# Optimization experiments

Hardware: AMD Instinct MI355X
Metric: run time of the kernel (lower is better)

## Reference

```python
import jax, jax.numpy as jnp
import numpy as np

N_HEADS = 16
SEG = 64
EPS = 1e-6


def _sigma(x):
    # ELU(x) + 1 kernel feature map (strictly positive)
    return jax.nn.elu(x) + 1.0


def setup_inputs() -> dict:
    key = jax.random.key(0)
    kx, kq, kk, kv, ko = jax.random.split(key, 5)
    B, T, D = 4, 4096, 1024
    scale = D ** -0.5
    return {
        "x": jax.random.normal(kx, (B, T, D), dtype=jnp.float32),
        "W_q": jax.random.normal(kq, (D, D), dtype=jnp.float32) * scale,
        "W_k": jax.random.normal(kk, (D, D), dtype=jnp.float32) * scale,
        "W_v": jax.random.normal(kv, (D, D), dtype=jnp.float32) * scale,
        "W_o": jax.random.normal(ko, (D, D), dtype=jnp.float32) * scale,
        "beta_param": jnp.zeros((N_HEADS,), dtype=jnp.float32),
    }


def _infini_attention(x, W_q, W_k, W_v, W_o, beta_param):
    B, T, D = x.shape
    H = N_HEADS
    dk = D // H
    assert T % SEG == 0
    S = T // SEG

    def proj(W):
        # nn.Linear: x @ W.T ; split heads -> (B,H,T,dk) -> (S,B,H,SEG,dk)
        y = (x @ W.T).reshape(B, T, H, dk).transpose(0, 2, 1, 3)
        return y.reshape(B, H, S, SEG, dk).transpose(2, 0, 1, 3, 4)

    Qs, Ks, Vs = proj(W_q), proj(W_k), proj(W_v)

    beta = jax.nn.sigmoid(beta_param).reshape(1, H, 1, 1)
    causal = jnp.triu(jnp.ones((SEG, SEG), dtype=bool), k=1)
    inv_sqrt_dk = 1.0 / jnp.sqrt(jnp.asarray(dk, x.dtype))

    M0 = jnp.zeros((B, H, dk, dk), dtype=x.dtype)
    z0 = jnp.zeros((B, H, dk), dtype=x.dtype)

    def step(carry, qkv):
        M, z = carry
        q, k, v = qkv  # each (B,H,SEG,dk)
        # Eq.4 memory retrieval
        sq = _sigma(q)
        denom_q = jnp.sum(sq * z[:, :, None, :], axis=-1, keepdims=True) + EPS
        A_mem = jnp.matmul(sq, M) / denom_q
        # local causal softmax attention
        scores = jnp.matmul(q, jnp.swapaxes(k, -2, -1)) * inv_sqrt_dk
        scores = jnp.where(causal, -jnp.inf, scores)
        A_dot = jnp.matmul(jax.nn.softmax(scores, axis=-1), v)
        A_s = beta * A_mem + (1.0 - beta) * A_dot
        # Eq.5 delta-rule memory update
        sk = _sigma(k)
        denom_k = jnp.sum(sk * z[:, :, None, :], axis=-1, keepdims=True) + EPS
        V_prev = jnp.matmul(sk, M) / denom_k
        M_new = M + jnp.einsum("bhtk,bhtv->bhkv", sk, v - V_prev)
        z_new = z + jnp.sum(sk, axis=-2)
        return (M_new, z_new), A_s

    (M, z), outs = jax.lax.scan(step, (M0, z0), (Qs, Ks, Vs))
    # outs: (S,B,H,SEG,dk) -> (B,T,D)
    out = outs.transpose(1, 3, 0, 2, 4).reshape(B, S * SEG, H, dk)
    # careful: need segment-major time ordering -> (B, H, T, dk) then (B,T,H,dk)
    out = outs.transpose(1, 2, 0, 3, 4).reshape(B, H, T, dk)
    out = out.transpose(0, 2, 1, 3).reshape(B, T, D)
    out = out @ W_o.T
    return out, M.mean(0), z.mean(0)


def reference(x, W_q, W_k, W_v, W_o, beta_param):
    return _infini_attention(x, W_q, W_k, W_v, W_o, beta_param)
```

## Files before the change

### kernel.cpp

```cpp
#include <hip/hip_runtime.h>

typedef __bf16 bf16_t;
typedef __bf16 bf16x8 __attribute__((ext_vector_type(8)));
typedef __bf16 bf16x4 __attribute__((ext_vector_type(4)));
typedef float  f32x4  __attribute__((ext_vector_type(4)));

#define QKV_STR 3072

__device__ __forceinline__ void gload16(const bf16_t* g, bf16_t* l) {
    __builtin_amdgcn_global_load_lds(
        (const __attribute__((address_space(1))) void*)(g),
        (__attribute__((address_space(3))) void*)(l), 16, 0, 0);
}

__global__ __launch_bounds__(256) void cast_bf16_kernel(const float* __restrict__ in,
                                                        bf16_t* __restrict__ out, int n4) {
    int i = blockIdx.x * 256 + threadIdx.x;
    if (i >= n4) return;
    f32x4 v = *reinterpret_cast<const f32x4*>(in + (size_t)i * 4);
    bf16x4 o;
    o[0] = (bf16_t)v[0]; o[1] = (bf16_t)v[1]; o[2] = (bf16_t)v[2]; o[3] = (bf16_t)v[3];
    *reinterpret_cast<bf16x4*>(out + (size_t)i * 4) = o;
}

__global__ __launch_bounds__(256) void cast4_kernel(const float* __restrict__ w0,
                                                    const float* __restrict__ w1,
                                                    const float* __restrict__ w2,
                                                    const float* __restrict__ w3,
                                                    bf16_t* __restrict__ o0,
                                                    bf16_t* __restrict__ o1,
                                                    bf16_t* __restrict__ o2,
                                                    bf16_t* __restrict__ o3) {
    int which = blockIdx.x >> 10;
    int i = (blockIdx.x & 1023) * 256 + threadIdx.x;
    const float* in = (which == 0) ? w0 : (which == 1) ? w1 : (which == 2) ? w2 : w3;
    bf16_t*     out = (which == 0) ? o0 : (which == 1) ? o1 : (which == 2) ? o2 : o3;
    f32x4 v = *reinterpret_cast<const f32x4*>(in + (size_t)i * 4);
    bf16x4 o;
    o[0] = (bf16_t)v[0]; o[1] = (bf16_t)v[1]; o[2] = (bf16_t)v[2]; o[3] = (bf16_t)v[3];
    *reinterpret_cast<bf16x4*>(out + (size_t)i * 4) = o;
}

__device__ __forceinline__ bf16x8 sigma8(bf16x8 x) {
    bf16x8 o;
#pragma unroll
    for (int j = 0; j < 8; j++) {
        float f = (float)x[j];
        float sg = f > 0.f ? f + 1.f : __expf(f);
        o[j] = (bf16_t)sg;
    }
    return o;
}

template <int OUT_BF16>
__global__ __launch_bounds__(512, 2) void gemm256(const bf16_t* __restrict__ A,
                                                  const bf16_t* __restrict__ Bm,
                                                  void* __restrict__ Cv,
                                                  int M, int N, int K) {
    __shared__ bf16_t As[4][256 * 32];
    __shared__ bf16_t Bs[4][256 * 32];

    int nbn = N >> 8;
    int nwg = (M >> 8) * nbn;
    int bid = blockIdx.x;
    int wg = ((nwg & 7) == 0) ? ((bid & 7) * (nwg >> 3) + (bid >> 3)) : bid;
    int bm = wg / nbn, bn = wg % nbn;

    int tid = threadIdx.x;
    int w = tid >> 6, lane = tid & 63;
    int wm = w >> 2, wn = w & 3;
    int lr = lane & 15, lk = lane >> 4;

    int srow = lane >> 2;
    int schunk = (lane & 3) ^ ((lane >> 3) & 3);
    const bf16_t* gA0 = A  + (size_t)(bm * 256 + w * 32 + srow) * K + schunk * 8;
    const bf16_t* gA1 = gA0 + (size_t)16 * K;
    const bf16_t* gB0 = Bm + (size_t)(bn * 256 + w * 32 + srow) * K + schunk * 8;
    const bf16_t* gB1 = gB0 + (size_t)16 * K;
    int lO0 = (w * 32) * 32 + lane * 8;
    int lO1 = (w * 32 + 16) * 32 + lane * 8;

    int chunkb = (lk ^ ((lr >> 1) & 3)) << 4;
    int aoff[8], boff[4];
#pragma unroll
    for (int mi = 0; mi < 8; mi++) aoff[mi] = (wm * 128 + mi * 16 + lr) * 64 + chunkb;
#pragma unroll
    for (int ni = 0; ni < 4; ni++) boff[ni] = (wn * 64 + ni * 16 + lr) * 64 + chunkb;

    f32x4 acc[8][4];
#pragma unroll
    for (int mi = 0; mi < 8; mi++)
#pragma unroll
        for (int ni = 0; ni < 4; ni++) acc[mi][ni] = (f32x4){0.f, 0.f, 0.f, 0.f};

    const int NT = K >> 5;

    auto STAGE = [&](int t) {
        int slot = t & 3;
        size_t ko = (size_t)t * 32;
        gload16(gA0 + ko, &As[slot][lO0]);
        gload16(gA1 + ko, &As[slot][lO1]);
        gload16(gB0 + ko, &Bs[slot][lO0]);
        gload16(gB1 + ko, &Bs[slot][lO1]);
    };

    STAGE(0); STAGE(1); STAGE(2);

#pragma unroll 1
    for (int t = 0; t < NT; ++t) {
        int ahead = NT - 1 - t;
        if (ahead >= 2)      asm volatile("s_waitcnt vmcnt(8)" ::: "memory");
        else if (ahead == 1) asm volatile("s_waitcnt vmcnt(4)" ::: "memory");
        else                 asm volatile("s_waitcnt vmcnt(0)" ::: "memory");
        __builtin_amdgcn_sched_barrier(0);
        __builtin_amdgcn_s_barrier();
        __builtin_amdgcn_sched_barrier(0);

        const char* pa = (const char*)(&As[t & 3][0]);
        const char* pb = (const char*)(&Bs[t & 3][0]);
        bf16x8 af[8], bfr[4];
#pragma unroll
        for (int ni = 0; ni < 4; ni++)
            bfr[ni] = *reinterpret_cast<const bf16x8*>(pb + boff[ni]);
#pragma unroll
        for (int mi = 0; mi < 8; mi++)
            af[mi] = *reinterpret_cast<const bf16x8*>(pa + aoff[mi]);

        if (t + 3 < NT) STAGE(t + 3);

        __builtin_amdgcn_s_setprio(1);
#pragma unroll
        for (int mi = 0; mi < 8; mi++)
#pragma unroll
            for (int ni = 0; ni < 4; ni++)
                acc[mi][ni] = __builtin_amdgcn_mfma_f32_16x16x32_bf16(af[mi], bfr[ni], acc[mi][ni], 0, 0, 0);
        __builtin_amdgcn_s_setprio(0);
    }

    int row0 = bm * 256 + wm * 128 + lk * 4;
    int col0 = bn * 256 + wn * 64 + lr;
#pragma unroll
    for (int mi = 0; mi < 8; mi++)
#pragma unroll
        for (int ni = 0; ni < 4; ni++)
#pragma unroll
            for (int jj = 0; jj < 4; jj++) {
                size_t idx = (size_t)(row0 + mi * 16 + jj) * N + (col0 + ni * 16);
                float v = acc[mi][ni][jj];
                if (OUT_BF16) reinterpret_cast<bf16_t*>(Cv)[idx] = (bf16_t)v;
                else          reinterpret_cast<float*>(Cv)[idx]  = v;
            }
}

__global__ __launch_bounds__(256) void attn_kernel(bf16_t* __restrict__ QKV,
                                                   bf16_t* __restrict__ skTg,
                                                   float* __restrict__ csum,
                                                   bf16_t* __restrict__ Adot) {
    __shared__ bf16_t kS[64 * 72];
    __shared__ bf16_t vS[64 * 72];
    __shared__ bf16_t skT[64 * 72];
    __shared__ bf16_t vT[64 * 72];
    __shared__ bf16_t pS[64 * 72];
    __shared__ float  scr[64 * 68];

    int u = blockIdx.x;
    int bh = u >> 6, s = u & 63;
    int b = bh >> 4, h = bh & 15;
    int tid = threadIdx.x;
    int w = tid >> 6, lane = tid & 63;
    int lr = lane & 15, lk = lane >> 4;
    int r = tid >> 2, qd = tid & 3, c0 = qd << 4;

    bf16_t* qp = QKV + (size_t)(b * 4096 + s * 64) * QKV_STR + (size_t)h * 64;
    bf16_t* kp = qp + 1024;
    bf16_t* vp = qp + 2048;
    size_t sb = ((size_t)bh * 64 + s) * 4096;

    {
        bf16x8 k0 = *reinterpret_cast<const bf16x8*>(kp + (size_t)r * QKV_STR + c0);
        bf16x8 k1 = *reinterpret_cast<const bf16x8*>(kp + (size_t)r * QKV_STR + c0 + 8);
        bf16x8 v0 = *reinterpret_cast<const bf16x8*>(vp + (size_t)r * QKV_STR + c0);
        bf16x8 v1 = *reinterpret_cast<const bf16x8*>(vp + (size_t)r * QKV_STR + c0 + 8);
        *reinterpret_cast<bf16x8*>(&kS[r * 72 + c0])     = k0;
        *reinterpret_cast<bf16x8*>(&kS[r * 72 + c0 + 8]) = k1;
        *reinterpret_cast<bf16x8*>(&vS[r * 72 + c0])     = v0;
        *reinterpret_cast<bf16x8*>(&vS[r * 72 + c0 + 8]) = v1;
        bf16x8 s0 = sigma8(k0), s1 = sigma8(k1);
        *reinterpret_cast<bf16x8*>(kp + (size_t)r * QKV_STR + c0)     = s0;
        *reinterpret_cast<bf16x8*>(kp + (size_t)r * QKV_STR + c0 + 8) = s1;
#pragma unroll
        for (int j = 0; j < 8; j++) {
            skT[(c0 + j) * 72 + r]     = s0[j];
            skT[(c0 + 8 + j) * 72 + r] = s1[j];
            vT[(c0 + j) * 72 + r]      = v0[j];
            vT[(c0 + 8 + j) * 72 + r]  = v1[j];
        }
    }
    __syncthreads();

    if (tid < 64) {
        float acc = 0.f;
#pragma unroll 8
        for (int t = 0; t < 64; t++) acc += (float)skT[tid * 72 + t];
        csum[((size_t)bh * 64 + s) * 64 + tid] = acc;
    }
    *reinterpret_cast<bf16x8*>(skTg + sb + (size_t)r * 64 + c0) =
        *reinterpret_cast<const bf16x8*>(&skT[r * 72 + c0]);
    *reinterpret_cast<bf16x8*>(skTg + sb + (size_t)r * 64 + c0 + 8) =
        *reinterpret_cast<const bf16x8*>(&skT[r * 72 + c0 + 8]);
    *reinterpret_cast<bf16x8*>(vp + (size_t)r * QKV_STR + c0) =
        *reinterpret_cast<const bf16x8*>(&vT[r * 72 + c0]);
    *reinterpret_cast<bf16x8*>(vp + (size_t)r * QKV_STR + c0 + 8) =
        *reinterpret_cast<const bf16x8*>(&vT[r * 72 + c0 + 8]);

    {
        bf16x8 aq[2];
#pragma unroll
        for (int ks = 0; ks < 2; ks++)
            aq[ks] = *reinterpret_cast<const bf16x8*>(qp + (size_t)(w * 16 + lr) * QKV_STR + lk * 8 + ks * 32);
        f32x4 sc[4];
#pragma unroll
        for (int ct = 0; ct < 4; ct++) {
            sc[ct] = (f32x4){0.f, 0.f, 0.f, 0.f};
#pragma unroll
            for (int ks = 0; ks < 2; ks++) {
                bf16x8 bfrag = *reinterpret_cast<const bf16x8*>(&kS[(ct * 16 + lr) * 72 + lk * 8 + ks * 32]);
                sc[ct] = __builtin_amdgcn_mfma_f32_16x16x32_bf16(aq[ks], bfrag, sc[ct], 0, 0, 0);
            }
        }
#pragma unroll
        for (int ct = 0; ct < 4; ct++)
#pragma unroll
            for (int j = 0; j < 4; j++)
                scr[(w * 16 + lk * 4 + j) * 68 + ct * 16 + lr] = sc[ct][j] * 0.125f;
    }
    __syncthreads();

    {
        float p[16];
        float mx = -3.4e38f;
        const float* srow_p = &scr[r * 68 + c0];
#pragma unroll
        for (int i = 0; i < 16; i++) {
            int c = c0 + i;
            float v = (c <= r) ? srow_p[i] : -3.4e38f;
            p[i] = v;
            mx = fmaxf(mx, v);
        }
        mx = fmaxf(mx, __shfl_xor(mx, 1));
        mx = fmaxf(mx, __shfl_xor(mx, 2));
        float sum = 0.f;
#pragma unroll
        for (int i = 0; i < 16; i++) {
            int c = c0 + i;
            float e = (c <= r) ? __expf(p[i] - mx) : 0.f;
            p[i] = e;
            sum += e;
        }
        sum += __shfl_xor(sum, 1);
        sum += __shfl_xor(sum, 2);
        float inv = 1.f / sum;
        bf16x8 p0, p1;
#pragma unroll
        for (int j = 0; j < 8; j++) {
            p0[j] = (bf16_t)(p[j] * inv);
            p1[j] = (bf16_t)(p[8 + j] * inv);
        }
        *reinterpret_cast<bf16x8*>(&pS[r * 72 + c0])     = p0;
        *reinterpret_cast<bf16x8*>(&pS[r * 72 + c0 + 8]) = p1;
    }
    __syncthreads();

    {
        f32x4 ad[4];
#pragma unroll
        for (int ct = 0; ct < 4; ct++) {
            ad[ct] = (f32x4){0.f, 0.f, 0.f, 0.f};
#pragma unroll
            for (int ks = 0; ks < 2; ks++) {
                bf16x8 afrag = *reinterpret_cast<const bf16x8*>(&pS[(w * 16 + lr) * 72 + lk * 8 + ks * 32]);
                bf16x8 bfrag = *reinterpret_cast<const bf16x8*>(&vT[(ct * 16 + lr) * 72 + lk * 8 + ks * 32]);
                ad[ct] = __builtin_amdgcn_mfma_f32_16x16x32_bf16(afrag, bfrag, ad[ct], 0, 0, 0);
            }
        }
#pragma unroll
        for (int ct = 0; ct < 4; ct++)
#pragma unroll
            for (int j = 0; j < 4; j++)
                kS[(w * 16 + lk * 4 + j) * 72 + ct * 16 + lr] = (bf16_t)ad[ct][j];
    }
    __syncthreads();
    *reinterpret_cast<bf16x8*>(Adot + sb + (size_t)r * 64 + c0) =
        *reinterpret_cast<const bf16x8*>(&kS[r * 72 + c0]);
    *reinterpret_cast<bf16x8*>(Adot + sb + (size_t)r * 64 + c0 + 8) =
        *reinterpret_cast<const bf16x8*>(&kS[r * 72 + c0 + 8]);
}

__global__ __launch_bounds__(64) void zprefix_kernel(const float* __restrict__ csum,
                                                     float* __restrict__ zx,
                                                     float* __restrict__ zfin) {
    int bh = blockIdx.x;
    int d = threadIdx.x;
    float c[64];
#pragma unroll
    for (int s = 0; s < 64; s++)
        c[s] = csum[((size_t)bh * 64 + s) * 64 + d];
    float z = 0.f;
#pragma unroll
    for (int s = 0; s < 64; s++) {
        zx[((size_t)bh * 64 + s) * 64 + d] = z;
        z += c[s];
    }
    zfin[bh * 64 + d] = z;
}

__global__ __launch_bounds__(64) void denomk_kernel(const bf16_t* __restrict__ QKV,
                                                    const float* __restrict__ zx,
                                                    float* __restrict__ invk) {
    __shared__ float zL[64];
    int u = blockIdx.x;
    int bh = u >> 6, s = u & 63;
    int b = bh >> 4, h = bh & 15;
    int tid = threadIdx.x;
    zL[tid] = zx[((size_t)bh * 64 + s) * 64 + tid];
    __syncthreads();
    const bf16_t* src = QKV + (size_t)(b * 4096 + s * 64 + tid) * QKV_STR +
                        (size_t)h * 64 + 1024;
    float acc = 0.f;
#pragma unroll
    for (int blk = 0; blk < 8; blk++) {
        bf16x8 v = *reinterpret_cast<const bf16x8*>(src + blk * 8);
#pragma unroll
        for (int j = 0; j < 8; j++)
            acc = __builtin_fmaf((float)v[j], zL[blk * 8 + j], acc);
    }
    invk[((size_t)bh * 64 + s) * 64 + tid] = 1.f / (acc + 1e-6f);
}

__global__ __launch_bounds__(64, 1) void scan_kernel(const bf16_t* __restrict__ QKV,
                                                     const bf16_t* __restrict__ skTg,
                                                     const float* __restrict__ invk,
                                                     bf16_t* __restrict__ Msnap,
                                                     float* __restrict__ Mfin) {
    __shared__ bf16_t MbL[16 * 72];
    __shared__ bf16_t uTL[16 * 72];
    __shared__ float  ikL[64];

    int blk = blockIdx.x;
    int bh = blk & 63, cq = blk >> 6;
    int c0 = cq << 4;
    int b = bh >> 4, h = bh & 15;
    int lane = threadIdx.x;
    int lr = lane & 15, lk = lane >> 4;
    int vr = lane >> 2, vt0 = (lane & 3) << 4;

    const bf16_t* sKb = QKV + 1024;
    const bf16_t* vTb = QKV + 2048;
    size_t chbase = (size_t)(b * 4096) * QKV_STR + (size_t)h * 64;
    size_t stbase = (size_t)bh * 64 * 4096;
    const size_t SEG = (size_t)64 * QKV_STR;

    auto swz = [](bf16_t* base, int row, int intra) -> bf16_t* {
        return (bf16_t*)((char*)base + row * 144 + (intra ^ ((row & 7) << 4)));
    };

    for (int i = lane; i < 16 * 72; i += 64) MbL[i] = (bf16_t)0.f;
    f32x4 Mreg[4];
#pragma unroll
    for (int rt = 0; rt < 4; rt++) Mreg[rt] = (f32x4){0.f, 0.f, 0.f, 0.f};

    bf16x8 cK[4][2], cT[4][2];
#pragma unroll
    for (int rt = 0; rt < 4; rt++)
#pragma unroll
        for (int ks = 0; ks < 2; ks++) {
            cK[rt][ks] = *reinterpret_cast<const bf16x8*>(
                sKb + chbase + (size_t)(rt * 16 + lr) * QKV_STR + lk * 8 + ks * 32);
            cT[rt][ks] = *reinterpret_cast<const bf16x8*>(
                skTg + stbase + (size_t)(rt * 16 + lr) * 64 + lk * 8 + ks * 32);
        }
    {
        bf16x8 v0 = *reinterpret_cast<const bf16x8*>(vTb + chbase + (size_t)(c0 + vr) * QKV_STR + vt0);
        bf16x8 v1 = *reinterpret_cast<const bf16x8*>(vTb + chbase + (size_t)(c0 + vr) * QKV_STR + vt0 + 8);
        *reinterpret_cast<bf16x8*>(swz(uTL, vr, vt0 * 2))      = v0;
        *reinterpret_cast<bf16x8*>(swz(uTL, vr, vt0 * 2 + 16)) = v1;
        ikL[lane] = invk[(size_t)bh * 4096 + lane];
    }

    for (int s = 0; s < 64; s++) {
        bf16x8 nK[4][2], nT[4][2], nv0, nv1;
        float nik = 0.f;
        if (s < 63) {
            size_t vs2 = chbase + (size_t)(s + 1) * SEG;
            size_t sb2 = stbase + (size_t)(s + 1) * 4096;
#pragma unroll
            for (int rt = 0; rt < 4; rt++)
#pragma unroll
                for (int ks = 0; ks < 2; ks++) {
                    nK[rt][ks] = *reinterpret_cast<const bf16x8*>(
                        sKb + vs2 + (size_t)(rt * 16 + lr) * QKV_STR + lk * 8 + ks * 32);
                    nT[rt][ks] = *reinterpret_cast<const bf16x8*>(
                        skTg + sb2 + (size_t)(rt * 16 + lr) * 64 + lk * 8 + ks * 32);
                }
            nv0 = *reinterpret_cast<const bf16x8*>(vTb + vs2 + (size_t)(c0 + vr) * QKV_STR + vt0);
            nv1 = *reinterpret_cast<const bf16x8*>(vTb + vs2 + (size_t)(c0 + vr) * QKV_STR + vt0 + 8);
            nik = invk[(size_t)bh * 4096 + (size_t)(s + 1) * 64 + lane];
        }

        bf16x8 mb0 = *reinterpret_cast<const bf16x8*>(swz(MbL, lr, lk * 16));
        bf16x8 mb1 = *reinterpret_cast<const bf16x8*>(swz(MbL, lr, lk * 16 + 64));
        f32x4 Y[4];
#pragma unroll
        for (int rt = 0; rt < 4; rt++) {
            Y[rt] = (f32x4){0.f, 0.f, 0.f, 0.f};
            Y[rt] = __builtin_amdgcn_mfma_f32_16x16x32_bf16(cK[rt][0], mb0, Y[rt], 0, 0, 0);
            Y[rt] = __builtin_amdgcn_mfma_f32_16x16x32_bf16(cK[rt][1], mb1, Y[rt], 0, 0, 0);
        }

#pragma unroll
        for (int rt = 0; rt < 4; rt++) {
            bf16x4 vv = *reinterpret_cast<const bf16x4*>(swz(uTL, lr, rt * 32 + lk * 8));
            bf16x4 uu;
#pragma unroll
            for (int j = 0; j < 4; j++) {
                float ik = ikL[rt * 16 + lk * 4 + j];
                uu[j] = (bf16_t)((float)vv[j] - Y[rt][j] * ik);
            }
            *reinterpret_cast<bf16x4*>(swz(uTL, lr, rt * 32 + lk * 8)) = uu;
        }

        bf16x8 ub0 = *reinterpret_cast<const bf16x8*>(swz(uTL, lr, lk * 16));
        bf16x8 ub1 = *reinterpret_cast<const bf16x8*>(swz(uTL, lr, lk * 16 + 64));
#pragma unroll
        for (int rt = 0; rt < 4; rt++) {
            Mreg[rt] = __builtin_amdgcn_mfma_f32_16x16x32_bf16(cT[rt][0], ub0, Mreg[rt], 0, 0, 0);
            Mreg[rt] = __builtin_amdgcn_mfma_f32_16x16x32_bf16(cT[rt][1], ub1, Mreg[rt], 0, 0, 0);
        }

#pragma unroll
        for (int rt = 0; rt < 4; rt++) {
            bf16x4 mp;
#pragma unroll
            for (int j = 0; j < 4; j++) mp[j] = (bf16_t)Mreg[rt][j];
            *reinterpret_cast<bf16x4*>(swz(MbL, lr, rt * 32 + lk * 8)) = mp;
            if (s < 63)
                *reinterpret_cast<bf16x4*>(
                    Msnap + (((size_t)bh * 64 + s + 1) * 64 + c0 + lr) * 64 + rt * 16 + lk * 4) = mp;
        }

        if (s < 63) {
#pragma unroll
            for (int rt = 0; rt < 4; rt++)
#pragma unroll
                for (int ks = 0; ks < 2; ks++) { cK[rt][ks] = nK[rt][ks]; cT[rt][ks] = nT[rt][ks]; }
            *reinterpret_cast<bf16x8*>(swz(uTL, vr, vt0 * 2))      = nv0;
            *reinterpret_cast<bf16x8*>(swz(uTL, vr, vt0 * 2 + 16)) = nv1;
            ikL[lane] = nik;
        }
    }

#pragma unroll
    for (int rt = 0; rt < 4; rt++)
#pragma unroll
        for (int j = 0; j < 4; j++)
            Mfin[(size_t)bh * 4096 + (size_t)(rt * 16 + lk * 4 + j) * 64 + c0 + lr] = Mreg[rt][j];
}

__global__ __launch_bounds__(256) void combine_kernel(const bf16_t* __restrict__ QKV,
                                                      const bf16_t* __restrict__ Msnap,
                                                      const bf16_t* __restrict__ Adot,
                                                      const float* __restrict__ zx,
                                                      const float* __restrict__ beta_param,
                                                      bf16_t* __restrict__ Op) {
    __shared__ bf16_t oS[64 * 72];
    __shared__ bf16_t adS[64 * 72];
    __shared__ float  iq[64];
    __shared__ float  zL[64];

    int u = blockIdx.x;
    int bh = u >> 6, s = u & 63;
    int b = bh >> 4, h = bh & 15;
    int tid = threadIdx.x;
    int w = tid >> 6, lane = tid & 63;
    int lr = lane & 15, lk = lane >> 4;
    int r = tid >> 2, c0 = (tid & 3) << 4;

    const bf16_t* qp = QKV + (size_t)(b * 4096 + s * 64) * QKV_STR + (size_t)h * 64;
    size_t vsegO = ((size_t)b * 4096 + s * 64) * 1024 + (size_t)h * 64;
    size_t sb = ((size_t)bh * 64 + s) * 4096;
    size_t ib = ((size_t)bh * 64 + s) * 64;

    float beta = 1.f / (1.f + __expf(-beta_param[h]));
    float omb = 1.f - beta;

    *reinterpret_cast<bf16x8*>(&adS[r * 72 + c0]) =
        *reinterpret_cast<const bf16x8*>(Adot + sb + (size_t)r * 64 + c0);
    *reinterpret_cast<bf16x8*>(&adS[r * 72 + c0 + 8]) =
        *reinterpret_cast<const bf16x8*>(Adot + sb + (size_t)r * 64 + c0 + 8);
    if (tid < 64) {
        zL[tid] = zx[ib + tid];
        iq[tid] = 0.f;
    }
    __syncthreads();

    f32x4 Y[4];
#pragma unroll
    for (int ct = 0; ct < 4; ct++) Y[ct] = (f32x4){0.f, 0.f, 0.f, 0.f};
    if (s > 0) {
        bf16x8 aq[2];
#pragma unroll
        for (int ks = 0; ks < 2; ks++)
            aq[ks] = sigma8(*reinterpret_cast<const bf16x8*>(
                qp + (size_t)(w * 16 + lr) * QKV_STR + lk * 8 + ks * 32));
        float dq = 0.f;
#pragma unroll
        for (int ks = 0; ks < 2; ks++)
#pragma unroll
            for (int j = 0; j < 8; j++)
                dq = __builtin_fmaf((float)aq[ks][j], zL[ks * 32 + lk * 8 + j], dq);
        dq += __shfl_xor(dq, 16);
        dq += __shfl_xor(dq, 32);
        if (lk == 0) iq[w * 16 + lr] = 1.f / (dq + 1e-6f);
#pragma unroll
        for (int ct = 0; ct < 4; ct++)
#pragma unroll
            for (int ks = 0; ks < 2; ks++) {
                bf16x8 bfrag = *reinterpret_cast<const bf16x8*>(
                    Msnap + sb + (size_t)(ct * 16 + lr) * 64 + lk * 8 + ks * 32);
                Y[ct] = __builtin_amdgcn_mfma_f32_16x16x32_bf16(aq[ks], bfrag, Y[ct], 0, 0, 0);
            }
    }
    __syncthreads();

#pragma unroll
    for (int ct = 0; ct < 4; ct++) {
        int colc = ct * 16 + lr;
#pragma unroll
        for (int j = 0; j < 4; j++) {
            int t = w * 16 + lk * 4 + j;
            float o = beta * (Y[ct][j] * iq[t]) + omb * (float)adS[t * 72 + colc];
            oS[t * 72 + colc] = (bf16_t)o;
        }
    }
    __syncthreads();

    *reinterpret_cast<bf16x8*>(Op + vsegO + (size_t)r * 1024 + c0) =
        *reinterpret_cast<const bf16x8*>(&oS[r * 72 + c0]);
    *reinterpret_cast<bf16x8*>(Op + vsegO + (size_t)r * 1024 + c0 + 8) =
        *reinterpret_cast<const bf16x8*>(&oS[r * 72 + c0 + 8]);
}

__global__ __launch_bounds__(256) void mean_kernel(const float* __restrict__ Mfin,
                                                   const float* __restrict__ zfin,
                                                   float* __restrict__ out) {
    int idx = blockIdx.x * 256 + threadIdx.x;
    if (idx < 65536) {
        out[16777216 + idx] = 0.25f * (Mfin[idx] + Mfin[idx + 65536] +
                                       Mfin[idx + 131072] + Mfin[idx + 196608]);
    } else if (idx < 66560) {
        int j = idx - 65536;
        out[16842752 + j] = 0.25f * (zfin[j] + zfin[j + 1024] + zfin[j + 2048] + zfin[j + 3072]);
    }
}

extern "C" void kernel_launch(void* const* d_in, const int* in_sizes, int n_in,
                              void* d_out, int out_size, void* d_ws, size_t ws_size,
                              hipStream_t stream) {
    const float* x      = (const float*)d_in[0];
    const float* Wq     = (const float*)d_in[1];
    const float* Wk     = (const float*)d_in[2];
    const float* Wv     = (const float*)d_in[3];
    const float* Wo     = (const float*)d_in[4];
    const float* beta_p = (const float*)d_in[5];
    float* out = (float*)d_out;
    char* ws = (char*)d_ws;

    const size_t NX = 16777216ull;

    bf16_t* xb   = (bf16_t*)ws;
    bf16_t* Adot = xb;
    bf16_t* Wqb  = (bf16_t*)(ws + 33554432);
    bf16_t* Wkb  = (bf16_t*)(ws + 35651584);
    bf16_t* Wvb  = (bf16_t*)(ws + 37748736);
    bf16_t* Wob  = (bf16_t*)(ws + 39845888);
    bf16_t* QKV  = (bf16_t*)(ws + 41943040);
    bf16_t* skT  = (bf16_t*)(ws + 142606336);
    bf16_t* Op   = (bf16_t*)(ws + 176160768);
    float*  csum = (float*)(ws + 209715200);
    float*  zx   = (float*)(ws + 210763776);
    float*  invk = (float*)(ws + 212860928);
    float*  Mfin = (float*)(ws + 213909504);
    float*  zfin = (float*)(ws + 214958080);
    bf16_t* Msnap = (bf16_t*)d_out;

    cast_bf16_kernel<<<dim3(16384), dim3(256), 0, stream>>>(x, xb, (int)(NX / 4));
    cast4_kernel<<<dim3(4096), dim3(256), 0, stream>>>(Wq, Wk, Wv, Wo, Wqb, Wkb, Wvb, Wob);

    gemm256<1><<<dim3(768), dim3(512), 0, stream>>>(xb, Wqb, (void*)QKV, 16384, 3072, 1024);

    attn_kernel<<<dim3(4096), dim3(256), 0, stream>>>(QKV, skT, csum, Adot);
    zprefix_kernel<<<dim3(64), dim3(64), 0, stream>>>(csum, zx, zfin);
    denomk_kernel<<<dim3(4096), dim3(64), 0, stream>>>(QKV, zx, invk);
    scan_kernel<<<dim3(256), dim3(64), 0, stream>>>(QKV, skT, invk, Msnap, Mfin);
    combine_kernel<<<dim3(4096), dim3(256), 0, stream>>>(QKV, Msnap, Adot, zx, beta_p, Op);

    gemm256<0><<<dim3(256), dim3(512), 0, stream>>>(Op, Wob, d_out, 16384, 1024, 1024);
    mean_kernel<<<dim3(260), dim3(256), 0, stream>>>(Mfin, zfin, out);
}
```

Baseline: 318.2 us.

## Precompute per-segment delta-rule operators to shorten the serial memory scan

The delta-rule update M += skᵀ(v - sk·M·invk) is rewritten as M = M - A·M + B. A = skᵀ·diag(invk)·sk and B = skᵀ·v are computed for every segment in a new, fully parallel prepA kernel. The serial scan then does one small MFMA product plus an elementwise update per step, instead of two dependent MFMA products with an LDS round trip for the intermediate u. The cost is an extra kernel that writes A in place over skT and B into spare output memory. It also adds bf16 rounding of the precomputed A and B, which may change accuracy.

```diff
diff --git a/kernel.cpp b/kernel.cpp
--- a/kernel.cpp
+++ b/kernel.cpp
@@ -337,28 +337,97 @@
     invk[((size_t)bh * 64 + s) * 64 + tid] = 1.f / (acc + 1e-6f);
 }
 
-__global__ __launch_bounds__(64, 1) void scan_kernel(const bf16_t* __restrict__ QKV,
-                                                     const bf16_t* __restrict__ skTg,
-                                                     const float* __restrict__ invk,
+__global__ __launch_bounds__(256) void prepA_kernel(const bf16_t* QKV,
+                                                    const bf16_t* skTg_in,
+                                                    const float* __restrict__ invk,
+                                                    bf16_t* Ag,
+                                                    bf16_t* __restrict__ bTg) {
+    __shared__ bf16_t tA[64 * 72];
+    __shared__ bf16_t tB[64 * 72];
+
+    int u = blockIdx.x;
+    int bh = u >> 6, s = u & 63;
+    int b = bh >> 4, h = bh & 15;
+    int tid = threadIdx.x;
+    int w = tid >> 6, lane = tid & 63;
+    int lr = lane & 15, lk = lane >> 4;
+    int r = tid >> 2, cc0 = (tid & 3) << 4;
+
+    size_t sb4 = (size_t)u * 4096;
+    size_t ib  = (size_t)u * 64;
+
+    bf16x8 aT[2], av[2], skB[4][2];
+    f32x4 iv[2][2];
+#pragma unroll
+    for (int ks = 0; ks < 2; ks++) {
+        aT[ks] = *reinterpret_cast<const bf16x8*>(
+            skTg_in + sb4 + (size_t)(w * 16 + lr) * 64 + lk * 8 + ks * 32);
+        av[ks] = *reinterpret_cast<const bf16x8*>(
+            QKV + (size_t)(b * 4096 + s * 64 + w * 16 + lr) * QKV_STR + (size_t)h * 64 + 2048 +
+            lk * 8 + ks * 32);
+        iv[ks][0] = *reinterpret_cast<const f32x4*>(invk + ib + ks * 32 + lk * 8);
+        iv[ks][1] = *reinterpret_cast<const f32x4*>(invk + ib + ks * 32 + lk * 8 + 4);
+    }
+#pragma unroll
+    for (int ct = 0; ct < 4; ct++)
+#pragma unroll
+        for (int ks = 0; ks < 2; ks++)
+            skB[ct][ks] = *reinterpret_cast<const bf16x8*>(
+                skTg_in + sb4 + (size_t)(ct * 16 + lr) * 64 + lk * 8 + ks * 32);
+
+    bf16x8 skS[4][2];
+#pragma unroll
+    for (int ct = 0; ct < 4; ct++)
+#pragma unroll
+        for (int ks = 0; ks < 2; ks++)
+#pragma unroll
+            for (int j = 0; j < 8; j++) {
+                float sc = (j < 4) ? iv[ks][0][j] : iv[ks][1][j - 4];
+                skS[ct][ks][j] = (bf16_t)((float)skB[ct][ks][j] * sc);
+            }
+
+    f32x4 Acc[4], Bcc[4];
+#pragma unroll
+    for (int ct = 0; ct < 4; ct++) {
+        Acc[ct] = (f32x4){0.f, 0.f, 0.f, 0.f};
+        Bcc[ct] = (f32x4){0.f, 0.f, 0.f, 0.f};
+        Acc[ct] = __builtin_amdgcn_mfma_f32_16x16x32_bf16(aT[0], skS[ct][0], Acc[ct], 0, 0, 0);
+        Acc[ct] = __builtin_amdgcn_mfma_f32_16x16x32_bf16(aT[1], skS[ct][1], Acc[ct], 0, 0, 0);
+        Bcc[ct] = __builtin_amdgcn_mfma_f32_16x16x32_bf16(av[0], skB[ct][0], Bcc[ct], 0, 0, 0);
+        Bcc[ct] = __builtin_amdgcn_mfma_f32_16x16x32_bf16(av[1], skB[ct][1], Bcc[ct], 0, 0, 0);
+    }
+
+#pragma unroll
+    for (int ct = 0; ct < 4; ct++)
+#pragma unroll
+        for (int j = 0; j < 4; j++) {
+            tA[(w * 16 + lk * 4 + j) * 72 + ct * 16 + lr] = (bf16_t)Acc[ct][j];
+            tB[(w * 16 + lk * 4 + j) * 72 + ct * 16 + lr] = (bf16_t)Bcc[ct][j];
+        }
+    __syncthreads();
+
+    *reinterpret_cast<bf16x8*>(Ag + sb4 + (size_t)r * 64 + cc0) =
+        *reinterpret_cast<const bf16x8*>(&tA[r * 72 + cc0]);
+    *reinterpret_cast<bf16x8*>(Ag + sb4 + (size_t)r * 64 + cc0 + 8) =
+        *reinterpret_cast<const bf16x8*>(&tA[r * 72 + cc0 + 8]);
+    *reinterpret_cast<bf16x8*>(bTg + sb4 + (size_t)r * 64 + cc0) =
+        *reinterpret_cast<const bf16x8*>(&tB[r * 72 + cc0]);
+    *reinterpret_cast<bf16x8*>(bTg + sb4 + (size_t)r * 64 + cc0 + 8) =
+        *reinterpret_cast<const bf16x8*>(&tB[r * 72 + cc0 + 8]);
+}
+
+__global__ __launch_bounds__(64, 1) void scan_kernel(const bf16_t* __restrict__ Ag,
+                                                     const bf16_t* __restrict__ bTg,
                                                      bf16_t* __restrict__ Msnap,
                                                      float* __restrict__ Mfin) {
     __shared__ bf16_t MbL[16 * 72];
-    __shared__ bf16_t uTL[16 * 72];
-    __shared__ float  ikL[64];
 
     int blk = blockIdx.x;
     int bh = blk & 63, cq = blk >> 6;
     int c0 = cq << 4;
-    int b = bh >> 4, h = bh & 15;
     int lane = threadIdx.x;
     int lr = lane & 15, lk = lane >> 4;
-    int vr = lane >> 2, vt0 = (lane & 3) << 4;
-
-    const bf16_t* sKb = QKV + 1024;
-    const bf16_t* vTb = QKV + 2048;
-    size_t chbase = (size_t)(b * 4096) * QKV_STR + (size_t)h * 64;
-    size_t stbase = (size_t)bh * 64 * 4096;
-    const size_t SEG = (size_t)64 * QKV_STR;
+    size_t tb = (size_t)bh * 64 * 4096;
 
     auto swz = [](bf16_t* base, int row, int intra) -> bf16_t* {
         return (bf16_t*)((char*)base + row * 144 + (intra ^ ((row & 7) << 4)));
@@ -369,73 +438,49 @@
 #pragma unroll
     for (int rt = 0; rt < 4; rt++) Mreg[rt] = (f32x4){0.f, 0.f, 0.f, 0.f};
 
-    bf16x8 cK[4][2], cT[4][2];
-#pragma unroll
-    for (int rt = 0; rt < 4; rt++)
-#pragma unroll
-        for (int ks = 0; ks < 2; ks++) {
-            cK[rt][ks] = *reinterpret_cast<const bf16x8*>(
-                sKb + chbase + (size_t)(rt * 16 + lr) * QKV_STR + lk * 8 + ks * 32);
-            cT[rt][ks] = *reinterpret_cast<const bf16x8*>(
-                skTg + stbase + (size_t)(rt * 16 + lr) * 64 + lk * 8 + ks * 32);
-        }
-    {
-        bf16x8 v0 = *reinterpret_cast<const bf16x8*>(vTb + chbase + (size_t)(c0 + vr) * QKV_STR + vt0);
-        bf16x8 v1 = *reinterpret_cast<const bf16x8*>(vTb + chbase + (size_t)(c0 + vr) * QKV_STR + vt0 + 8);
-        *reinterpret_cast<bf16x8*>(swz(uTL, vr, vt0 * 2))      = v0;
-        *reinterpret_cast<bf16x8*>(swz(uTL, vr, vt0 * 2 + 16)) = v1;
-        ikL[lane] = invk[(size_t)bh * 4096 + lane];
+    bf16x8 cA[4][2];
+    bf16x4 cb[4];
+#pragma unroll
+    for (int rt = 0; rt < 4; rt++) {
+#pragma unroll
+        for (int ks = 0; ks < 2; ks++)
+            cA[rt][ks] = *reinterpret_cast<const bf16x8*>(
+                Ag + tb + (size_t)(rt * 16 + lr) * 64 + lk * 8 + ks * 32);
+        cb[rt] = *reinterpret_cast<const bf16x4*>(
+            bTg + tb + (size_t)(c0 + lr) * 64 + rt * 16 + lk * 4);
     }
 
     for (int s = 0; s < 64; s++) {
-        bf16x8 nK[4][2], nT[4][2], nv0, nv1;
-        float nik = 0.f;
+        bf16x8 nA[4][2];
+        bf16x4 nb[4];
         if (s < 63) {
-            size_t vs2 = chbase + (size_t)(s + 1) * SEG;
-            size_t sb2 = stbase + (size_t)(s + 1) * 4096;
-#pragma unroll
-            for (int rt = 0; rt < 4; rt++)
-#pragma unroll
-                for (int ks = 0; ks < 2; ks++) {
-                    nK[rt][ks] = *reinterpret_cast<const bf16x8*>(
-                        sKb + vs2 + (size_t)(rt * 16 + lr) * QKV_STR + lk * 8 + ks * 32);
-                    nT[rt][ks] = *reinterpret_cast<const bf16x8*>(
-                        skTg + sb2 + (size_t)(rt * 16 + lr) * 64 + lk * 8 + ks * 32);
-                }
-            nv0 = *reinterpret_cast<const bf16x8*>(vTb + vs2 + (size_t)(c0 + vr) * QKV_STR + vt0);
-            nv1 = *reinterpret_cast<const bf16x8*>(vTb + vs2 + (size_t)(c0 + vr) * QKV_STR + vt0 + 8);
-            nik = invk[(size_t)bh * 4096 + (size_t)(s + 1) * 64 + lane];
+            size_t t2 = tb + (size_t)(s + 1) * 4096;
+#pragma unroll
+            for (int rt = 0; rt < 4; rt++) {
+#pragma unroll
+                for (int ks = 0; ks < 2; ks++)
+                    nA[rt][ks] = *reinterpret_cast<const bf16x8*>(
+                        Ag + t2 + (size_t)(rt * 16 + lr) * 64 + lk * 8 + ks * 32);
+                nb[rt] = *reinterpret_cast<const bf16x4*>(
+                    bTg + t2 + (size_t)(c0 + lr) * 64 + rt * 16 + lk * 4);
+            }
         }
 
         bf16x8 mb0 = *reinterpret_cast<const bf16x8*>(swz(MbL, lr, lk * 16));
         bf16x8 mb1 = *reinterpret_cast<const bf16x8*>(swz(MbL, lr, lk * 16 + 64));
-        f32x4 Y[4];
+        f32x4 G[4];
 #pragma unroll
         for (int rt = 0; rt < 4; rt++) {
-            Y[rt] = (f32x4){0.f, 0.f, 0.f, 0.f};
-            Y[rt] = __builtin_amdgcn_mfma_f32_16x16x32_bf16(cK[rt][0], mb0, Y[rt], 0, 0, 0);
-            Y[rt] = __builtin_amdgcn_mfma_f32_16x16x32_bf16(cK[rt][1], mb1, Y[rt], 0, 0, 0);
-        }
-
-#pragma unroll
-        for (int rt = 0; rt < 4; rt++) {
-            bf16x4 vv = *reinterpret_cast<const bf16x4*>(swz(uTL, lr, rt * 32 + lk * 8));
-            bf16x4 uu;
-#pragma unroll
-            for (int j = 0; j < 4; j++) {
-                float ik = ikL[rt * 16 + lk * 4 + j];
-                uu[j] = (bf16_t)((float)vv[j] - Y[rt][j] * ik);
-            }
-            *reinterpret_cast<bf16x4*>(swz(uTL, lr, rt * 32 + lk * 8)) = uu;
-        }
-
-        bf16x8 ub0 = *reinterpret_cast<const bf16x8*>(swz(uTL, lr, lk * 16));
-        bf16x8 ub1 = *reinterpret_cast<const bf16x8*>(swz(uTL, lr, lk * 16 + 64));
-#pragma unroll
-        for (int rt = 0; rt < 4; rt++) {
-            Mreg[rt] = __builtin_amdgcn_mfma_f32_16x16x32_bf16(cT[rt][0], ub0, Mreg[rt], 0, 0, 0);
-            Mreg[rt] = __builtin_amdgcn_mfma_f32_16x16x32_bf16(cT[rt][1], ub1, Mreg[rt], 0, 0, 0);
-        }
+            G[rt] = (f32x4){0.f, 0.f, 0.f, 0.f};
+            G[rt] = __builtin_amdgcn_mfma_f32_16x16x32_bf16(cA[rt][0], mb0, G[rt], 0, 0, 0);
+            G[rt] = __builtin_amdgcn_mfma_f32_16x16x32_bf16(cA[rt][1], mb1, G[rt], 0, 0, 0);
+        }
+
+#pragma unroll
+        for (int rt = 0; rt < 4; rt++)
+#pragma unroll
+            for (int j = 0; j < 4; j++)
+                Mreg[rt][j] = Mreg[rt][j] - G[rt][j] + (float)cb[rt][j];
 
 #pragma unroll
         for (int rt = 0; rt < 4; rt++) {
@@ -450,12 +495,11 @@
 
         if (s < 63) {
 #pragma unroll
-            for (int rt = 0; rt < 4; rt++)
-#pragma unroll
-                for (int ks = 0; ks < 2; ks++) { cK[rt][ks] = nK[rt][ks]; cT[rt][ks] = nT[rt][ks]; }
-            *reinterpret_cast<bf16x8*>(swz(uTL, vr, vt0 * 2))      = nv0;
-            *reinterpret_cast<bf16x8*>(swz(uTL, vr, vt0 * 2 + 16)) = nv1;
-            ikL[lane] = nik;
+            for (int rt = 0; rt < 4; rt++) {
+#pragma unroll
+                for (int ks = 0; ks < 2; ks++) cA[rt][ks] = nA[rt][ks];
+                cb[rt] = nb[rt];
+            }
         }
     }
 
@@ -592,6 +636,7 @@
     float*  Mfin = (float*)(ws + 213909504);
     float*  zfin = (float*)(ws + 214958080);
     bf16_t* Msnap = (bf16_t*)d_out;
+    bf16_t* bTg   = (bf16_t*)d_out + 16777216;
 
     cast_bf16_kernel<<<dim3(16384), dim3(256), 0, stream>>>(x, xb, (int)(NX / 4));
     cast4_kernel<<<dim3(4096), dim3(256), 0, stream>>>(Wq, Wk, Wv, Wo, Wqb, Wkb, Wvb, Wob);
@@ -601,7 +646,8 @@
     attn_kernel<<<dim3(4096), dim3(256), 0, stream>>>(QKV, skT, csum, Adot);
     zprefix_kernel<<<dim3(64), dim3(64), 0, stream>>>(csum, zx, zfin);
     denomk_kernel<<<dim3(4096), dim3(64), 0, stream>>>(QKV, zx, invk);
-    scan_kernel<<<dim3(256), dim3(64), 0, stream>>>(QKV, skT, invk, Msnap, Mfin);
+    prepA_kernel<<<dim3(4096), dim3(256), 0, stream>>>(QKV, skT, invk, skT, bTg);
+    scan_kernel<<<dim3(256), dim3(64), 0, stream>>>(skT, bTg, Msnap, Mfin);
     combine_kernel<<<dim3(4096), dim3(256), 0, stream>>>(QKV, Msnap, Adot, zx, beta_p, Op);
 
     gemm256<0><<<dim3(256), dim3(512), 0, stream>>>(Op, Wob, d_out, 16384, 1024, 1024);
```

After: 336.9 us. 1.06x slower.
